# Kernel optimization log

Measured on AMD Instinct MI355X. Metric: run time of the kernel, lower is better.

Reference implementation:

```python
import jax, jax.numpy as jnp
import numpy as np

Q, A, R, S, K = 256, 28, 512, 256, 2  # n_quantize, n_aux, n_resch, n_skipch, kernel_size
DEPTH, REPEAT = 10, 3
L = DEPTH * REPEAT  # 30 layers
T = 8192


def setup_inputs() -> dict:
    key = jax.random.key(0)
    ks = jax.random.split(key, 24)
    w = lambda k, shape: jax.random.normal(k, shape, dtype=jnp.float32) * 0.05
    return {
        "x": jax.random.randint(ks[0], (1, T), 0, Q, dtype=jnp.int32),
        "h": jax.random.normal(ks[1], (1, A, T), dtype=jnp.float32),
        "Wc": w(ks[2], (R, Q, K)), "bc": w(ks[3], (R,)),
        "Wds": w(ks[4], (L, R, R, K)), "bds": w(ks[5], (L, R)),
        "Wdt": w(ks[6], (L, R, R, K)), "bdt": w(ks[7], (L, R)),
        "Was": w(ks[8], (L, R, A, 1)), "bas": w(ks[9], (L, R)),
        "Wat": w(ks[10], (L, R, A, 1)), "bat": w(ks[11], (L, R)),
        "Wsk": w(ks[12], (L, S, R, 1)), "bsk": w(ks[13], (L, S)),
        "Wr": w(ks[14], (L, R, R, 1)), "br": w(ks[15], (L, R)),
        "Wp1": w(ks[16], (S, S, 1)), "bp1": w(ks[17], (S,)),
        "Wp2": w(ks[18], (Q, S, 1)), "bp2": w(ks[19], (Q,)),
    }


def _cconv(z, w, b, d):
    # causal dilated conv: z [1,C,T], w [O,C,K] -> [1,O,T]
    pad = (w.shape[2] - 1) * d
    y = jax.lax.conv_general_dilated(
        z, w, window_strides=(1,), padding=[(pad, 0)], rhs_dilation=(d,),
        dimension_numbers=("NCH", "OIH", "NCH"))
    return y + b[None, :, None]


def reference(x, h, Wc, bc, Wds, bds, Wdt, bdt, Was, bas, Wat, bat,
              Wsk, bsk, Wr, br, Wp1, bp1, Wp2, bp2):
    dilations = [2 ** i for i in range(DEPTH)] * REPEAT
    oh = jax.nn.one_hot(x, Q, dtype=Wc.dtype).transpose(0, 2, 1)  # [1,Q,T]
    out = _cconv(oh, Wc, bc, 1)  # [1,R,T]
    skip_sum = jnp.zeros((1, S, oh.shape[2]), dtype=Wc.dtype)
    for l, d in enumerate(dilations):
        s = _cconv(out, Wds[l], bds[l], d) + _cconv(h, Was[l], bas[l], 1)
        t = _cconv(out, Wdt[l], bdt[l], d) + _cconv(h, Wat[l], bat[l], 1)
        g = jax.nn.sigmoid(s) * jnp.tanh(t)  # gated activation
        skip_sum = skip_sum + _cconv(g, Wsk[l], bsk[l], 1)
        out = _cconv(g, Wr[l], br[l], 1) + out  # residual
    o = jax.nn.relu(skip_sum)
    o = jax.nn.relu(_cconv(o, Wp1, bp1, 1))
    o = _cconv(o, Wp2, bp2, 1)  # [1,Q,T]
    return o[0].T  # [T,Q], matches squeeze(0).transpose(0,1)
```

## Files before the change

kernel.cpp:

```cpp
#include <hip/hip_runtime.h>
#include <hip/hip_bf16.h>
#include <math.h>
#include <stdint.h>

#define T_LEN 8192
#define RCH   512
#define SCH   256
#define QCH   256
#define ACH   28
#define NLAYER 30
#define KGATE 1088
#define KSR   512
#define KPOST 256

typedef _Float16 f16x8 __attribute__((ext_vector_type(8)));
typedef float    f32x4 __attribute__((ext_vector_type(4)));

#define SB0() __builtin_amdgcn_sched_barrier(0)

static __device__ __forceinline__ unsigned short f2h(float v) {
    _Float16 h = (_Float16)v;
    return *reinterpret_cast<unsigned short*>(&h);
}

static __device__ __forceinline__ float fsig(float x) {
    return __builtin_amdgcn_rcpf(1.f + __expf(-x));
}

#define G2L(SRC, DST) __builtin_amdgcn_global_load_lds(                        \
    (__attribute__((address_space(1))) void*)(const void*)(SRC),              \
    (__attribute__((address_space(3))) void*)(void*)(DST), 16, 0, 0)

__global__ void pack_gate_v(const float* __restrict__ Wds,
                            const float* __restrict__ Wdt,
                            const float* __restrict__ Was,
                            const float* __restrict__ Wat,
                            unsigned short* __restrict__ dst) {
    int l = blockIdx.y;
    int c = blockIdx.x * 256 + threadIdx.x;
    int tile = c >> 6, lane = c & 63;
    int mt = tile / 34, kt = tile % 34;
    int m  = mt * 16 + (lane & 15);
    int k0 = kt * 32 + (lane >> 4) * 8;
    int br = m & 1, ch = m >> 1;
    const float* Wd = (br ? Wdt : Wds) + (size_t)l * RCH * RCH * 2;
    const float* Wa = (br ? Wat : Was) + (size_t)l * RCH * ACH;
    unsigned short o[8];
    if (k0 < 512) {
        const float* base = Wd + ((size_t)ch * 512 + k0) * 2;
        #pragma unroll
        for (int q = 0; q < 4; ++q) {
            float4 v = *(const float4*)(base + q * 4);
            o[q * 2 + 0] = f2h(v.x);
            o[q * 2 + 1] = f2h(v.z);
        }
    } else if (k0 < 1024) {
        const float* base = Wd + ((size_t)ch * 512 + (k0 - 512)) * 2;
        #pragma unroll
        for (int q = 0; q < 4; ++q) {
            float4 v = *(const float4*)(base + q * 4);
            o[q * 2 + 0] = f2h(v.y);
            o[q * 2 + 1] = f2h(v.w);
        }
    } else {
        int a0 = k0 - 1024;
        #pragma unroll
        for (int i = 0; i < 8; ++i)
            o[i] = (a0 + i < ACH) ? f2h(Wa[(size_t)ch * ACH + a0 + i]) : (unsigned short)0;
    }
    *(uint4*)&dst[(size_t)l * 1024 * KGATE + (size_t)tile * 512 + lane * 8] = *(uint4*)o;
}

__global__ void pack_sr_v(const float* __restrict__ Wsk,
                          const float* __restrict__ Wr,
                          unsigned short* __restrict__ dst) {
    int l = blockIdx.y;
    int c = blockIdx.x * 256 + threadIdx.x;
    int tile = c >> 6, lane = c & 63;
    int mt = tile >> 4, kt = tile & 15;
    int m  = mt * 16 + (lane & 15);
    int k0 = kt * 32 + (lane >> 4) * 8;
    const float* row = (m < SCH) ? (Wsk + (size_t)l * SCH * RCH + (size_t)m * 512)
                                 : (Wr  + (size_t)l * RCH * RCH + (size_t)(m - SCH) * 512);
    float4 v0 = *(const float4*)(row + k0);
    float4 v1 = *(const float4*)(row + k0 + 4);
    unsigned short o[8] = { f2h(v0.x), f2h(v0.y), f2h(v0.z), f2h(v0.w),
                            f2h(v1.x), f2h(v1.y), f2h(v1.z), f2h(v1.w) };
    *(uint4*)&dst[(size_t)l * 768 * KSR + (size_t)tile * 512 + lane * 8] = *(uint4*)o;
}

__global__ void pack_post_v(const float* __restrict__ W,
                            unsigned short* __restrict__ dst) {
    int c = blockIdx.x * 256 + threadIdx.x;
    int tile = c >> 6, lane = c & 63;
    int mt = tile >> 3, kt = tile & 7;
    int m  = mt * 16 + (lane & 15);
    int k0 = kt * 32 + (lane >> 4) * 8;
    float4 v0 = *(const float4*)(W + (size_t)m * 256 + k0);
    float4 v1 = *(const float4*)(W + (size_t)m * 256 + k0 + 4);
    unsigned short o[8] = { f2h(v0.x), f2h(v0.y), f2h(v0.z), f2h(v0.w),
                            f2h(v1.x), f2h(v1.y), f2h(v1.z), f2h(v1.w) };
    *(uint4*)&dst[(size_t)tile * 512 + lane * 8] = *(uint4*)o;
}

__global__ void transpose_wc(const float* __restrict__ Wc,
                             float* __restrict__ WcT) {
    int idx = blockIdx.x * 256 + threadIdx.x;
    int r = idx >> 9;
    int qt = idx & 511;
    int q = qt >> 1, tap = qt & 1;
    WcT[(size_t)q * 1024 + tap * 512 + r] = Wc[(size_t)r * 512 + qt];
}

__global__ void embed_v(const int* __restrict__ x,
                        const float* __restrict__ WcT,
                        const float* __restrict__ bc,
                        float* __restrict__ out_tm,
                        unsigned short* __restrict__ outhf) {
    int idx = blockIdx.x * 256 + threadIdx.x;
    int t = idx >> 6, rc = (idx & 63) * 8;
    int x1 = x[t];
    const float* w1 = WcT + (size_t)x1 * 1024 + 512 + rc;
    float4 a = *(const float4*)w1;
    float4 b = *(const float4*)(w1 + 4);
    float4 c0 = *(const float4*)(bc + rc);
    float4 c1 = *(const float4*)(bc + rc + 4);
    a.x += c0.x; a.y += c0.y; a.z += c0.z; a.w += c0.w;
    b.x += c1.x; b.y += c1.y; b.z += c1.z; b.w += c1.w;
    if (t > 0) {
        const float* w0 = WcT + (size_t)x[t - 1] * 1024 + rc;
        float4 d0 = *(const float4*)w0;
        float4 d1 = *(const float4*)(w0 + 4);
        a.x += d0.x; a.y += d0.y; a.z += d0.z; a.w += d0.w;
        b.x += d1.x; b.y += d1.y; b.z += d1.z; b.w += d1.w;
    }
    size_t o = (size_t)t * 512 + rc;
    *(float4*)&out_tm[o] = a;
    *(float4*)&out_tm[o + 4] = b;
    unsigned short p[8] = { f2h(a.x), f2h(a.y), f2h(a.z), f2h(a.w),
                            f2h(b.x), f2h(b.y), f2h(b.z), f2h(b.w) };
    *(uint4*)&outhf[o + 512 * 512] = *(uint4*)p;
}

__global__ void packh_kernel(const float* __restrict__ h,
                             unsigned short* __restrict__ h_tm) {
    int idx = blockIdx.x * 256 + threadIdx.x;
    int t = idx >> 6, a = idx & 63;
    h_tm[idx] = f2h(a < ACH ? h[(size_t)a * T_LEN + t] : 0.f);
}

__global__ void reluconv_v(const float* __restrict__ skip,
                           unsigned short* __restrict__ dst) {
    int idx = (blockIdx.x * 256 + threadIdx.x) * 8;
    float4 v0 = *(const float4*)(skip + idx);
    float4 v1 = *(const float4*)(skip + idx + 4);
    unsigned short o[8] = { f2h(fmaxf(v0.x, 0.f)), f2h(fmaxf(v0.y, 0.f)),
                            f2h(fmaxf(v0.z, 0.f)), f2h(fmaxf(v0.w, 0.f)),
                            f2h(fmaxf(v1.x, 0.f)), f2h(fmaxf(v1.y, 0.f)),
                            f2h(fmaxf(v1.z, 0.f)), f2h(fmaxf(v1.w, 0.f)) };
    *(uint4*)&dst[idx] = *(uint4*)o;
}

template<int MODE, int KT64, int MB>
__global__ __launch_bounds__(256) void mfma_gemm(
    const unsigned short* __restrict__ Apk,
    const unsigned short* __restrict__ B0,
    const unsigned short* __restrict__ B2,
    const float* __restrict__ bias0, const float* __restrict__ bias1,
    const float* __restrict__ bias2, const float* __restrict__ bias3,
    float* __restrict__ O0, float* __restrict__ O1,
    unsigned short* __restrict__ OB, int dil)
{
    constexpr int KT32 = KT64 * 2;
    constexpr int NWG = MB * 64;
    constexpr int CPX = NWG / 8;

    __shared__ unsigned short Bsm[2][128 * 64];

    const int tid  = threadIdx.x;
    const int lane = tid & 63, wave = tid >> 6;
    const int wm = wave & 1, wn = wave >> 1;

    const int bid = blockIdx.x;
    const int swz = (bid & 7) * CPX + (bid >> 3);
    const int mb  = swz % MB;
    const int tb  = swz / MB;
    const int m0  = mb * 128;
    const int t0  = tb * 128;

    const int kc   = ((lane & 7) ^ (lane >> 3)) * 8;
    const int rsub = lane >> 3;

    const size_t mt0 = (size_t)(mb * 8) + wm * 4;

    f32x4 acc[4][4];
    #pragma unroll
    for (int a = 0; a < 4; ++a)
        #pragma unroll
        for (int b = 0; b < 4; ++b) acc[a][b] = (f32x4){0.f, 0.f, 0.f, 0.f};

    f16x8 afrA[4][2], afrB[4][2], bfr[4][2];

    auto stage_tile = [&](int kt, int buf) {
        const int kb = kt * 64;
        #pragma unroll
        for (int j = 0; j < 4; ++j) {
            const int row = wave * 32 + j * 8 + rsub;
            const int tg  = t0 + row;
            const unsigned short* src;
            if constexpr (MODE == 0) {
                if (kb < 512)
                    src = B0 + (size_t)(512 + tg - dil) * 512 + kb + kc;
                else if (kb < 1024)
                    src = B0 + (size_t)(512 + tg) * 512 + (kb - 512) + kc;
                else
                    src = B2 + (size_t)tg * 64 + kc;
            } else if constexpr (MODE == 1) {
                src = B0 + (size_t)tg * 512 + kb + kc;
            } else {
                src = B0 + (size_t)tg * 256 + kb + kc;
            }
            G2L(src, &Bsm[buf][(wave * 4 + j) * 512]);
        }
    };

    auto load_afr = [&](int kt, f16x8 (&dst)[4][2]) {
        #pragma unroll
        for (int mi = 0; mi < 4; ++mi)
            #pragma unroll
            for (int ks = 0; ks < 2; ++ks)
                dst[mi][ks] = *(const f16x8*)(Apk +
                    ((mt0 + mi) * KT32 + (size_t)(kt * 2 + ks)) * 512 + lane * 8);
    };

    auto load_bfr = [&](int buf) {
        #pragma unroll
        for (int ni = 0; ni < 4; ++ni)
            #pragma unroll
            for (int ks = 0; ks < 2; ++ks) {
                const int trow = wn * 64 + ni * 16 + (lane & 15);
                const int kch  = ks * 4 + (lane >> 4);
                const int sch  = kch ^ (lane & 7);
                bfr[ni][ks] = *(const f16x8*)&Bsm[buf][trow * 64 + sch * 8];
            }
    };

    auto do_mfma = [&](f16x8 (&A)[4][2]) {
        __builtin_amdgcn_s_setprio(1);
        #pragma unroll
        for (int mi = 0; mi < 4; ++mi)
            #pragma unroll
            for (int ni = 0; ni < 4; ++ni) {
                acc[mi][ni] = __builtin_amdgcn_mfma_f32_16x16x32_f16(
                    A[mi][0], bfr[ni][0], acc[mi][ni], 0, 0, 0);
                acc[mi][ni] = __builtin_amdgcn_mfma_f32_16x16x32_f16(
                    A[mi][1], bfr[ni][1], acc[mi][ni], 0, 0, 0);
            }
        __builtin_amdgcn_s_setprio(0);
    };

    stage_tile(0, 0);
    SB0();
    load_afr(0, afrA);
    SB0();
    asm volatile("s_waitcnt vmcnt(8)" ::: "memory");
    SB0();
    __builtin_amdgcn_s_barrier();

    #pragma unroll
    for (int kt = 0; kt < KT64; ++kt) {
        const int cur = kt & 1;
        if (kt + 1 < KT64) {
            stage_tile(kt + 1, cur ^ 1);
            SB0();
            if (cur) load_afr(kt + 1, afrA);
            else     load_afr(kt + 1, afrB);
            SB0();
        }
        load_bfr(cur);
        if (cur) do_mfma(afrB);
        else     do_mfma(afrA);
        if (kt + 1 < KT64) {
            SB0();
            asm volatile("s_waitcnt vmcnt(8) lgkmcnt(0)" ::: "memory");
            SB0();
            __builtin_amdgcn_s_barrier();
        }
    }

    const int rb0 = (lane >> 4) * 4;
    #pragma unroll
    for (int mi = 0; mi < 4; ++mi) {
        #pragma unroll
        for (int ni = 0; ni < 4; ++ni) {
            int m = m0 + wm * 64 + mi * 16 + rb0;
            int t = t0 + wn * 64 + ni * 16 + (lane & 15);
            f32x4 v = acc[mi][ni];
            if constexpr (MODE == 0) {
                int c0 = m >> 1;
                float s0 = v.x + bias0[c0]     + bias2[c0];
                float tv0 = v.y + bias1[c0]     + bias3[c0];
                float s1 = v.z + bias0[c0 + 1] + bias2[c0 + 1];
                float tv1 = v.w + bias1[c0 + 1] + bias3[c0 + 1];
                float g0 = fsig(s0) * (2.f * fsig(2.f * tv0) - 1.f);
                float g1 = fsig(s1) * (2.f * fsig(2.f * tv1) - 1.f);
                unsigned int p = (unsigned int)f2h(g0) | ((unsigned int)f2h(g1) << 16);
                *(unsigned int*)&OB[(size_t)t * 512 + c0] = p;
            } else if constexpr (MODE == 1) {
                if (m < SCH) {
                    float4* p = (float4*)&O0[(size_t)t * 256 + m];
                    float4 o = *p;
                    o.x += v.x + bias0[m + 0];
                    o.y += v.y + bias0[m + 1];
                    o.z += v.z + bias0[m + 2];
                    o.w += v.w + bias0[m + 3];
                    *p = o;
                } else {
                    int c = m - SCH;
                    float4* p = (float4*)&O1[(size_t)t * 512 + c];
                    float4 o = *p;
                    o.x += v.x + bias1[c + 0];
                    o.y += v.y + bias1[c + 1];
                    o.z += v.z + bias1[c + 2];
                    o.w += v.w + bias1[c + 3];
                    *p = o;
                    uint2 pk;
                    pk.x = (unsigned int)f2h(o.x) | ((unsigned int)f2h(o.y) << 16);
                    pk.y = (unsigned int)f2h(o.z) | ((unsigned int)f2h(o.w) << 16);
                    *(uint2*)&OB[(size_t)(512 + t) * 512 + c] = pk;
                }
            } else if constexpr (MODE == 2) {
                float o0 = fmaxf(v.x + bias0[m + 0], 0.f);
                float o1 = fmaxf(v.y + bias0[m + 1], 0.f);
                float o2 = fmaxf(v.z + bias0[m + 2], 0.f);
                float o3 = fmaxf(v.w + bias0[m + 3], 0.f);
                uint2 pk;
                pk.x = (unsigned int)f2h(o0) | ((unsigned int)f2h(o1) << 16);
                pk.y = (unsigned int)f2h(o2) | ((unsigned int)f2h(o3) << 16);
                *(uint2*)&OB[(size_t)t * 256 + m] = pk;
            } else {
                float4 o;
                o.x = v.x + bias0[m + 0];
                o.y = v.y + bias0[m + 1];
                o.z = v.z + bias0[m + 2];
                o.w = v.w + bias0[m + 3];
                *(float4*)&O0[(size_t)t * 256 + m] = o;
            }
        }
    }
}

extern "C" void kernel_launch(void* const* d_in, const int* in_sizes, int n_in,
                              void* d_out, int out_size, void* d_ws, size_t ws_size,
                              hipStream_t stream) {
    const int*   x   = (const int*)  d_in[0];
    const float* h   = (const float*)d_in[1];
    const float* Wc  = (const float*)d_in[2];
    const float* bc  = (const float*)d_in[3];
    const float* Wds = (const float*)d_in[4];
    const float* bds = (const float*)d_in[5];
    const float* Wdt = (const float*)d_in[6];
    const float* bdt = (const float*)d_in[7];
    const float* Was = (const float*)d_in[8];
    const float* bas = (const float*)d_in[9];
    const float* Wat = (const float*)d_in[10];
    const float* bat = (const float*)d_in[11];
    const float* Wsk = (const float*)d_in[12];
    const float* bsk = (const float*)d_in[13];
    const float* Wr  = (const float*)d_in[14];
    const float* br  = (const float*)d_in[15];
    const float* Wp1 = (const float*)d_in[16];
    const float* bp1 = (const float*)d_in[17];
    const float* Wp2 = (const float*)d_in[18];
    const float* bp2 = (const float*)d_in[19];
    float* dout = (float*)d_out;

    const size_t WG_EL  = (size_t)1024 * KGATE;
    const size_t WSR_EL = (size_t)768 * KSR;
    char* w = (char*)d_ws;
    float*          out_tm = (float*)w;               w += (size_t)T_LEN * 512 * 4;
    unsigned short* outhf  = (unsigned short*)w;      w += (size_t)(T_LEN + 512) * 512 * 2;
    unsigned short* g_tm   = (unsigned short*)w;      w += (size_t)T_LEN * 512 * 2;
    unsigned short* h_tm   = (unsigned short*)w;      w += (size_t)T_LEN * 64 * 2;
    unsigned short* skiphf = (unsigned short*)w;      w += (size_t)T_LEN * 256 * 2;
    unsigned short* o1hf   = (unsigned short*)w;      w += (size_t)T_LEN * 256 * 2;
    unsigned short* Wp1_pk = (unsigned short*)w;      w += (size_t)256 * 256 * 2;
    unsigned short* Wp2_pk = (unsigned short*)w;      w += (size_t)256 * 256 * 2;
    float*          WcT    = (float*)w;               w += (size_t)QCH * 2 * RCH * 4;
    unsigned short* Wg_pk  = (unsigned short*)w;
    size_t used_base = (size_t)((char*)Wg_pk - (char*)d_ws);
    size_t need_bulk = used_base + (WG_EL + WSR_EL) * NLAYER * 2;
    const bool bulk = ws_size >= need_bulk;
    unsigned short* Wsr_pk = Wg_pk + (bulk ? WG_EL * NLAYER : WG_EL);
    float* skip = dout;

    hipMemsetAsync(skip, 0, (size_t)T_LEN * 256 * 4, stream);
    hipMemsetAsync(outhf, 0, (size_t)512 * 512 * 2, stream);

    transpose_wc<<<1024, 256, 0, stream>>>(Wc, WcT);
    embed_v<<<(T_LEN * 64) / 256, 256, 0, stream>>>(x, WcT, bc, out_tm, outhf);
    packh_kernel<<<(T_LEN * 64) / 256, 256, 0, stream>>>(h, h_tm);
    pack_post_v<<<32, 256, 0, stream>>>(Wp1, Wp1_pk);
    pack_post_v<<<32, 256, 0, stream>>>(Wp2, Wp2_pk);

    if (bulk) {
        pack_gate_v<<<dim3(544, NLAYER), 256, 0, stream>>>(Wds, Wdt, Was, Wat, Wg_pk);
        pack_sr_v<<<dim3(192, NLAYER), 256, 0, stream>>>(Wsk, Wr, Wsr_pk);
    }

    for (int l = 0; l < NLAYER; ++l) {
        int dil = 1 << (l % 10);
        const unsigned short* wg;
        const unsigned short* wsr;
        if (bulk) {
            wg  = Wg_pk  + (size_t)l * WG_EL;
            wsr = Wsr_pk + (size_t)l * WSR_EL;
        } else {
            pack_gate_v<<<dim3(544, 1), 256, 0, stream>>>(
                Wds + (size_t)l * RCH * RCH * 2, Wdt + (size_t)l * RCH * RCH * 2,
                Was + (size_t)l * RCH * ACH, Wat + (size_t)l * RCH * ACH, Wg_pk);
            pack_sr_v<<<dim3(192, 1), 256, 0, stream>>>(
                Wsk + (size_t)l * SCH * RCH, Wr + (size_t)l * RCH * RCH, Wsr_pk);
            wg = Wg_pk; wsr = Wsr_pk;
        }
        mfma_gemm<0, KGATE / 64, 8><<<512, 256, 0, stream>>>(
            wg, outhf, h_tm,
            bds + (size_t)l * RCH, bdt + (size_t)l * RCH,
            bas + (size_t)l * RCH, bat + (size_t)l * RCH,
            nullptr, nullptr, g_tm, dil);
        mfma_gemm<1, KSR / 64, 6><<<384, 256, 0, stream>>>(
            wsr, g_tm, nullptr,
            bsk + (size_t)l * SCH, br + (size_t)l * RCH, nullptr, nullptr,
            skip, out_tm, outhf, 0);
    }

    reluconv_v<<<(T_LEN * 256 / 8) / 256, 256, 0, stream>>>(skip, skiphf);
    mfma_gemm<2, KPOST / 64, 2><<<128, 256, 0, stream>>>(
        Wp1_pk, skiphf, nullptr, bp1, nullptr, nullptr, nullptr,
        nullptr, nullptr, o1hf, 0);
    mfma_gemm<3, KPOST / 64, 2><<<128, 256, 0, stream>>>(
        Wp2_pk, o1hf, nullptr, bp2, nullptr, nullptr, nullptr,
        dout, nullptr, nullptr, 0);
}
```

Measured before the change: 1.545 ms.

## Repartition GEMM waves to 32x128 tiles and split gate weight packing

The MFMA GEMM wave layout changes from a 2x2 grid of 64x64 subtiles to four waves each covering 32 rows by all 128 time columns. Each wave now loads half as many A fragments from global memory and reads the full B tile from LDS, so the wait counts are adjusted to match. The gate weight packing kernel is split into a dilated-conv part that reads each float4 once and writes both taps, plus a separate small aux-weight kernel, which removes the duplicate strided reads. The new layout trades lower global A traffic for more LDS B reads per wave.

```diff
diff --git a/kernel.cpp b/kernel.cpp
--- a/kernel.cpp
+++ b/kernel.cpp
@@ -31,44 +31,54 @@
     (__attribute__((address_space(1))) void*)(const void*)(SRC),              \
     (__attribute__((address_space(3))) void*)(void*)(DST), 16, 0, 0)
 
-__global__ void pack_gate_v(const float* __restrict__ Wds,
-                            const float* __restrict__ Wdt,
-                            const float* __restrict__ Was,
-                            const float* __restrict__ Wat,
-                            unsigned short* __restrict__ dst) {
+__global__ void pack_gated_v(const float* __restrict__ Wds,
+                             const float* __restrict__ Wdt,
+                             unsigned short* __restrict__ dst) {
     int l = blockIdx.y;
     int c = blockIdx.x * 256 + threadIdx.x;
-    int tile = c >> 6, lane = c & 63;
-    int mt = tile / 34, kt = tile % 34;
-    int m  = mt * 16 + (lane & 15);
-    int k0 = kt * 32 + (lane >> 4) * 8;
+    int mlow = c & 15;
+    int kg   = (c >> 4) & 63;
+    int mhi  = c >> 10;
+    int m  = mhi * 16 + mlow;
+    int k0 = kg * 8;
     int br = m & 1, ch = m >> 1;
-    const float* Wd = (br ? Wdt : Wds) + (size_t)l * RCH * RCH * 2;
-    const float* Wa = (br ? Wat : Was) + (size_t)l * RCH * ACH;
+    const float* Wd = (br ? Wdt : Wds) + (size_t)l * RCH * RCH * 2
+                    + ((size_t)ch * 512 + k0) * 2;
+    unsigned short o0[8], o1[8];
+    #pragma unroll
+    for (int q = 0; q < 4; ++q) {
+        float4 v = *(const float4*)(Wd + q * 4);
+        o0[q * 2 + 0] = f2h(v.x); o1[q * 2 + 0] = f2h(v.y);
+        o0[q * 2 + 1] = f2h(v.z); o1[q * 2 + 1] = f2h(v.w);
+    }
+    int mt   = m >> 4;
+    int lane = ((k0 & 31) >> 3) * 16 + mlow;
+    int kt0  = k0 >> 5;
+    size_t base = (size_t)l * 1024 * KGATE;
+    *(uint4*)&dst[base + (size_t)(mt * 34 + kt0)      * 512 + lane * 8] = *(uint4*)o0;
+    *(uint4*)&dst[base + (size_t)(mt * 34 + kt0 + 16) * 512 + lane * 8] = *(uint4*)o1;
+}
+
+__global__ void pack_gatea_v(const float* __restrict__ Was,
+                             const float* __restrict__ Wat,
+                             unsigned short* __restrict__ dst) {
+    int l = blockIdx.y;
+    int c = blockIdx.x * 256 + threadIdx.x;
+    int mlow = c & 15;
+    int kg   = (c >> 4) & 7;
+    int mhi  = c >> 7;
+    int m  = mhi * 16 + mlow;
+    int a0 = kg * 8;
+    int br = m & 1, ch = m >> 1;
+    const float* Wa = (br ? Wat : Was) + (size_t)l * RCH * ACH + (size_t)ch * ACH;
     unsigned short o[8];
-    if (k0 < 512) {
-        const float* base = Wd + ((size_t)ch * 512 + k0) * 2;
-        #pragma unroll
-        for (int q = 0; q < 4; ++q) {
-            float4 v = *(const float4*)(base + q * 4);
-            o[q * 2 + 0] = f2h(v.x);
-            o[q * 2 + 1] = f2h(v.z);
-        }
-    } else if (k0 < 1024) {
-        const float* base = Wd + ((size_t)ch * 512 + (k0 - 512)) * 2;
-        #pragma unroll
-        for (int q = 0; q < 4; ++q) {
-            float4 v = *(const float4*)(base + q * 4);
-            o[q * 2 + 0] = f2h(v.y);
-            o[q * 2 + 1] = f2h(v.w);
-        }
-    } else {
-        int a0 = k0 - 1024;
-        #pragma unroll
-        for (int i = 0; i < 8; ++i)
-            o[i] = (a0 + i < ACH) ? f2h(Wa[(size_t)ch * ACH + a0 + i]) : (unsigned short)0;
-    }
-    *(uint4*)&dst[(size_t)l * 1024 * KGATE + (size_t)tile * 512 + lane * 8] = *(uint4*)o;
+    #pragma unroll
+    for (int i = 0; i < 8; ++i)
+        o[i] = (a0 + i < ACH) ? f2h(Wa[a0 + i]) : (unsigned short)0;
+    int mt   = m >> 4;
+    int lane = ((a0 & 31) >> 3) * 16 + mlow;
+    *(uint4*)&dst[(size_t)l * 1024 * KGATE
+                  + (size_t)(mt * 34 + 32 + (a0 >> 5)) * 512 + lane * 8] = *(uint4*)o;
 }
 
 __global__ void pack_sr_v(const float* __restrict__ Wsk,
@@ -179,7 +189,6 @@
 
     const int tid  = threadIdx.x;
     const int lane = tid & 63, wave = tid >> 6;
-    const int wm = wave & 1, wn = wave >> 1;
 
     const int bid = blockIdx.x;
     const int swz = (bid & 7) * CPX + (bid >> 3);
@@ -191,15 +200,15 @@
     const int kc   = ((lane & 7) ^ (lane >> 3)) * 8;
     const int rsub = lane >> 3;
 
-    const size_t mt0 = (size_t)(mb * 8) + wm * 4;
-
-    f32x4 acc[4][4];
+    const size_t mt0 = (size_t)(mb * 8) + wave * 2;
+
+    f32x4 acc[2][8];
     #pragma unroll
-    for (int a = 0; a < 4; ++a)
-        #pragma unroll
-        for (int b = 0; b < 4; ++b) acc[a][b] = (f32x4){0.f, 0.f, 0.f, 0.f};
-
-    f16x8 afrA[4][2], afrB[4][2], bfr[4][2];
+    for (int a = 0; a < 2; ++a)
+        #pragma unroll
+        for (int b = 0; b < 8; ++b) acc[a][b] = (f32x4){0.f, 0.f, 0.f, 0.f};
+
+    f16x8 afrA[2][2], afrB[2][2], bfr[8][2];
 
     auto stage_tile = [&](int kt, int buf) {
         const int kb = kt * 64;
@@ -224,9 +233,9 @@
         }
     };
 
-    auto load_afr = [&](int kt, f16x8 (&dst)[4][2]) {
-        #pragma unroll
-        for (int mi = 0; mi < 4; ++mi)
+    auto load_afr = [&](int kt, f16x8 (&dst)[2][2]) {
+        #pragma unroll
+        for (int mi = 0; mi < 2; ++mi)
             #pragma unroll
             for (int ks = 0; ks < 2; ++ks)
                 dst[mi][ks] = *(const f16x8*)(Apk +
@@ -235,22 +244,22 @@
 
     auto load_bfr = [&](int buf) {
         #pragma unroll
-        for (int ni = 0; ni < 4; ++ni)
+        for (int ni = 0; ni < 8; ++ni)
             #pragma unroll
             for (int ks = 0; ks < 2; ++ks) {
-                const int trow = wn * 64 + ni * 16 + (lane & 15);
+                const int trow = ni * 16 + (lane & 15);
                 const int kch  = ks * 4 + (lane >> 4);
                 const int sch  = kch ^ (lane & 7);
                 bfr[ni][ks] = *(const f16x8*)&Bsm[buf][trow * 64 + sch * 8];
             }
     };
 
-    auto do_mfma = [&](f16x8 (&A)[4][2]) {
+    auto do_mfma = [&](f16x8 (&A)[2][2]) {
         __builtin_amdgcn_s_setprio(1);
         #pragma unroll
-        for (int mi = 0; mi < 4; ++mi)
+        for (int mi = 0; mi < 2; ++mi)
             #pragma unroll
-            for (int ni = 0; ni < 4; ++ni) {
+            for (int ni = 0; ni < 8; ++ni) {
                 acc[mi][ni] = __builtin_amdgcn_mfma_f32_16x16x32_f16(
                     A[mi][0], bfr[ni][0], acc[mi][ni], 0, 0, 0);
                 acc[mi][ni] = __builtin_amdgcn_mfma_f32_16x16x32_f16(
@@ -263,7 +272,7 @@
     SB0();
     load_afr(0, afrA);
     SB0();
-    asm volatile("s_waitcnt vmcnt(8)" ::: "memory");
+    asm volatile("s_waitcnt vmcnt(4)" ::: "memory");
     SB0();
     __builtin_amdgcn_s_barrier();
 
@@ -282,7 +291,7 @@
         else     do_mfma(afrA);
         if (kt + 1 < KT64) {
             SB0();
-            asm volatile("s_waitcnt vmcnt(8) lgkmcnt(0)" ::: "memory");
+            asm volatile("s_waitcnt vmcnt(4) lgkmcnt(0)" ::: "memory");
             SB0();
             __builtin_amdgcn_s_barrier();
         }
@@ -290,11 +299,11 @@
 
     const int rb0 = (lane >> 4) * 4;
     #pragma unroll
-    for (int mi = 0; mi < 4; ++mi) {
-        #pragma unroll
-        for (int ni = 0; ni < 4; ++ni) {
-            int m = m0 + wm * 64 + mi * 16 + rb0;
-            int t = t0 + wn * 64 + ni * 16 + (lane & 15);
+    for (int mi = 0; mi < 2; ++mi) {
+        #pragma unroll
+        for (int ni = 0; ni < 8; ++ni) {
+            int m = m0 + wave * 32 + mi * 16 + rb0;
+            int t = t0 + ni * 16 + (lane & 15);
             f32x4 v = acc[mi][ni];
             if constexpr (MODE == 0) {
                 int c0 = m >> 1;
@@ -404,7 +413,8 @@
     pack_post_v<<<32, 256, 0, stream>>>(Wp2, Wp2_pk);
 
     if (bulk) {
-        pack_gate_v<<<dim3(544, NLAYER), 256, 0, stream>>>(Wds, Wdt, Was, Wat, Wg_pk);
+        pack_gated_v<<<dim3(256, NLAYER), 256, 0, stream>>>(Wds, Wdt, Wg_pk);
+        pack_gatea_v<<<dim3(32, NLAYER), 256, 0, stream>>>(Was, Wat, Wg_pk);
         pack_sr_v<<<dim3(192, NLAYER), 256, 0, stream>>>(Wsk, Wr, Wsr_pk);
     }
 
@@ -416,8 +426,9 @@
             wg  = Wg_pk  + (size_t)l * WG_EL;
             wsr = Wsr_pk + (size_t)l * WSR_EL;
         } else {
-            pack_gate_v<<<dim3(544, 1), 256, 0, stream>>>(
-                Wds + (size_t)l * RCH * RCH * 2, Wdt + (size_t)l * RCH * RCH * 2,
+            pack_gated_v<<<dim3(256, 1), 256, 0, stream>>>(
+                Wds + (size_t)l * RCH * RCH * 2, Wdt + (size_t)l * RCH * RCH * 2, Wg_pk);
+            pack_gatea_v<<<dim3(32, 1), 256, 0, stream>>>(
                 Was + (size_t)l * RCH * ACH, Wat + (size_t)l * RCH * ACH, Wg_pk);
             pack_sr_v<<<dim3(192, 1), 256, 0, stream>>>(
                 Wsk + (size_t)l * SCH * RCH, Wr + (size_t)l * RCH * RCH, Wsr_pk);
```

Result: faster. 1.427 ms, median of 2 (-7.6%).
